# Optimization experiments

Hardware: AMD Instinct MI355X
Metric: run time of the kernel (lower is better)

Reference implementation:

```python
import jax, jax.numpy as jnp
import numpy as np

M, N, K, B = 256, 1024, 16, 16384
P = [50] * K          # topk support size per iteration
EPS = 0.1             # epsilon in g(x)


def g(x):
    # adaptive threshold gate: 1 / (x/eps + 1)
    return 1.0 / (x / EPS + 1.0)


def soft_threshold(x, theta, p):
    # x, theta: [N, B]; keep entries above the p-th largest |x| per column,
    # soft-threshold the rest.
    abs_ = jnp.abs(x)
    st = jnp.sign(x) * jnp.maximum(abs_ - theta, 0.0)
    if p == 0:
        return st
    topk_vals, _ = jax.lax.top_k(abs_.T, p)      # [B, p], sorted descending
    thr = topk_vals[:, -1]                        # p-th largest per column -> [B]
    keep = (abs_ > thr[None, :]).astype(x.dtype)  # strict >, matching torch
    return keep * x + (1.0 - keep) * st


def setup_inputs() -> dict:
    key = jax.random.key(0)
    k1, k2, k3 = jax.random.split(key, 3)
    y = jax.random.normal(k1, (B, M), jnp.float32)
    phi = jax.random.normal(k2, (M, N), jnp.float32) / np.sqrt(M)
    W = jax.random.normal(k3, (M, N), jnp.float32) / np.sqrt(M)
    gamma = jnp.full((K,), 0.5, jnp.float32)
    theta = jnp.full((K,), 0.5, jnp.float32)
    info = jnp.zeros((1,), jnp.int32)  # unused by forward, pass-through arg
    return {"y": y, "phi": phi, "W": W, "gamma": gamma, "theta": theta, "info": info}


def reference(y, phi, W, gamma, theta, info):
    # y: [B, M]; phi, W: [M, N]; gamma, theta: [K]
    x = jnp.zeros((N, y.shape[0]), y.dtype)  # [N, B]
    yT = y.T                                  # [M, B]
    for i in range(K):
        c = W.T @ (phi @ x - yT)              # [N, B]
        th = theta[i] * g(jnp.abs(x))
        x = soft_threshold(x - gamma[i] * c, th, P[i])
    return (x.T, jnp.zeros((K, 1), x.dtype), jnp.zeros((K, 1), x.dtype))
```

## Files before the change

kernel.cpp:

```cpp
#include <hip/hip_runtime.h>
#include <hip/hip_bf16.h>
#include <cstdint>

#define NB 16384
#define NM 256
#define NN 1024
#define NITER 16
#define TOPK 50

typedef __attribute__((ext_vector_type(8))) short short8;
typedef __attribute__((ext_vector_type(4))) float f32x4;

__device__ inline unsigned short f2bf(float x) {
    unsigned u = __float_as_uint(x);
    return (unsigned short)((u + 0x7FFFu + ((u >> 16) & 1u)) >> 16);
}
__device__ inline float bf2f(unsigned short h) {
    return __uint_as_float(((unsigned)h) << 16);
}
__device__ inline void gload16(const void* g, void* lds) {
    __builtin_amdgcn_global_load_lds(
        (const __attribute__((address_space(1))) unsigned*)g,
        (__attribute__((address_space(3))) unsigned*)lds, 16, 0, 0);
}

__global__ __launch_bounds__(256) void split_phi_kernel(const float* __restrict__ phi,
                                                        unsigned short* __restrict__ h,
                                                        unsigned short* __restrict__ l) {
    int i = blockIdx.x * 256 + threadIdx.x;
    float v = phi[i];
    unsigned short hh = f2bf(v);
    h[i] = hh;
    l[i] = f2bf(v - bf2f(hh));
}

__global__ __launch_bounds__(256) void transpose_split_W(const float* __restrict__ W,
                                                         unsigned short* __restrict__ th,
                                                         unsigned short* __restrict__ tl) {
    __shared__ float tile[32][33];
    int n0 = blockIdx.x * 32;
    int m0 = blockIdx.y * 32;
    int tx = threadIdx.x;
    int ty = threadIdx.y;
    #pragma unroll
    for (int i = 0; i < 32; i += 8)
        tile[ty + i][tx] = W[(size_t)(m0 + ty + i) * NN + n0 + tx];
    __syncthreads();
    #pragma unroll
    for (int i = 0; i < 32; i += 8) {
        float v = tile[tx][ty + i];
        unsigned short hh = f2bf(v);
        size_t idx = (size_t)(n0 + ty + i) * NM + m0 + tx;
        th[idx] = hh;
        tl[idx] = f2bf(v - bf2f(hh));
    }
}

#define BM1 128
#define BN1 64
#define BK  32
__global__ __launch_bounds__(256) void gemm1_mfma(const unsigned short* __restrict__ Xh,
                                                  const unsigned short* __restrict__ Xl,
                                                  const unsigned short* __restrict__ Ph,
                                                  const unsigned short* __restrict__ Pl,
                                                  const float* __restrict__ y,
                                                  unsigned short* __restrict__ Rth,
                                                  unsigned short* __restrict__ Rtl) {
    __shared__ unsigned short sAh[BM1 * BK];
    __shared__ unsigned short sAl[BM1 * BK];
    __shared__ unsigned short sBh[BN1 * BK];
    __shared__ unsigned short sBl[BN1 * BK];

    const int tid = threadIdx.x, wave = tid >> 6, lane = tid & 63;
    const int b0 = blockIdx.x * BM1, n0 = blockIdx.y * BN1;
    const int wm = (wave & 1) * 64, wn = (wave >> 1) * 32;
    const int row16 = lane & 15, quad = lane >> 4;

    f32x4 acc[4][2];
    #pragma unroll
    for (int i = 0; i < 4; i++)
        #pragma unroll
        for (int j = 0; j < 2; j++) acc[i][j] = (f32x4){0.f, 0.f, 0.f, 0.f};

    for (int k0 = 0; k0 < NN; k0 += BK) {
        #pragma unroll
        for (int c = 0; c < 2; ++c) {
            int o = (wave * 2 + c) * 1024 + lane * 16;
            int row = o >> 6, colb = o & 63;
            size_t g = (size_t)(b0 + row) * NN + k0 + (colb >> 1);
            gload16(&Xh[g], (char*)sAh + o);
            gload16(&Xl[g], (char*)sAl + o);
        }
        {
            int o = wave * 1024 + lane * 16;
            int nrow = o >> 6, colb = o & 63;
            size_t g = (size_t)(n0 + nrow) * NN + k0 + (colb >> 1);
            gload16(&Ph[g], (char*)sBh + o);
            gload16(&Pl[g], (char*)sBl + o);
        }
        __syncthreads();
        short8 a[4], bh[2], bl[2];
        #pragma unroll
        for (int j = 0; j < 2; ++j) {
            int off = (wn + j * 16 + row16) * 64 + quad * 16;
            bh[j] = *(const short8*)((const char*)sBh + off);
            bl[j] = *(const short8*)((const char*)sBl + off);
        }
        #pragma unroll
        for (int i = 0; i < 4; ++i)
            a[i] = *(const short8*)((const char*)sAh + (wm + i * 16 + row16) * 64 + quad * 16);
        #pragma unroll
        for (int i = 0; i < 4; ++i)
            #pragma unroll
            for (int j = 0; j < 2; ++j) {
                acc[i][j] = __builtin_amdgcn_mfma_f32_16x16x32_bf16(a[i], bh[j], acc[i][j], 0, 0, 0);
                acc[i][j] = __builtin_amdgcn_mfma_f32_16x16x32_bf16(a[i], bl[j], acc[i][j], 0, 0, 0);
            }
        #pragma unroll
        for (int i = 0; i < 4; ++i)
            a[i] = *(const short8*)((const char*)sAl + (wm + i * 16 + row16) * 64 + quad * 16);
        #pragma unroll
        for (int i = 0; i < 4; ++i)
            #pragma unroll
            for (int j = 0; j < 2; ++j)
                acc[i][j] = __builtin_amdgcn_mfma_f32_16x16x32_bf16(a[i], bh[j], acc[i][j], 0, 0, 0);
        __syncthreads();
    }
    #pragma unroll
    for (int i = 0; i < 4; ++i)
        #pragma unroll
        for (int j = 0; j < 2; ++j)
            #pragma unroll
            for (int r = 0; r < 4; ++r) {
                int gm = b0 + wm + i * 16 + quad * 4 + r;
                int gn = n0 + wn + j * 16 + row16;
                size_t idx = (size_t)gm * NM + gn;
                float v = acc[i][j][r] - y[idx];
                unsigned short h = f2bf(v);
                Rth[idx] = h;
                Rtl[idx] = f2bf(v - bf2f(h));
            }
}

#define BM2 128
#define BN2 128
__global__ __launch_bounds__(256) void gemm2_mfma(const unsigned short* __restrict__ Rth,
                                                  const unsigned short* __restrict__ Rtl,
                                                  const unsigned short* __restrict__ Wth,
                                                  const unsigned short* __restrict__ Wtl,
                                                  const unsigned short* __restrict__ Xh,
                                                  const unsigned short* __restrict__ Xl,
                                                  const float* __restrict__ gamma,
                                                  int it,
                                                  float* __restrict__ V) {
    __shared__ unsigned short sAh[BM2 * BK];
    __shared__ unsigned short sAl[BM2 * BK];
    __shared__ unsigned short sBh[BN2 * BK];
    __shared__ unsigned short sBl[BN2 * BK];

    const int tid = threadIdx.x, wave = tid >> 6, lane = tid & 63;
    const int b0 = blockIdx.x * BM2, n0 = blockIdx.y * BN2;
    const int wm = (wave & 1) * 64, wn = (wave >> 1) * 64;
    const int row16 = lane & 15, quad = lane >> 4;

    f32x4 acc[4][4];
    #pragma unroll
    for (int i = 0; i < 4; i++)
        #pragma unroll
        for (int j = 0; j < 4; j++) acc[i][j] = (f32x4){0.f, 0.f, 0.f, 0.f};

    for (int k0 = 0; k0 < NM; k0 += BK) {
        #pragma unroll
        for (int c = 0; c < 2; ++c) {
            int o = (wave * 2 + c) * 1024 + lane * 16;
            int row = o >> 6, colb = o & 63;
            size_t gA = (size_t)(b0 + row) * NM + k0 + (colb >> 1);
            gload16(&Rth[gA], (char*)sAh + o);
            gload16(&Rtl[gA], (char*)sAl + o);
            size_t gB = (size_t)(n0 + row) * NM + k0 + (colb >> 1);
            gload16(&Wth[gB], (char*)sBh + o);
            gload16(&Wtl[gB], (char*)sBl + o);
        }
        __syncthreads();
        short8 a[4], bh[4], bl[4];
        #pragma unroll
        for (int j = 0; j < 4; ++j) {
            int off = (wn + j * 16 + row16) * 64 + quad * 16;
            bh[j] = *(const short8*)((const char*)sBh + off);
            bl[j] = *(const short8*)((const char*)sBl + off);
        }
        #pragma unroll
        for (int i = 0; i < 4; ++i)
            a[i] = *(const short8*)((const char*)sAh + (wm + i * 16 + row16) * 64 + quad * 16);
        #pragma unroll
        for (int i = 0; i < 4; ++i)
            #pragma unroll
            for (int j = 0; j < 4; ++j) {
                acc[i][j] = __builtin_amdgcn_mfma_f32_16x16x32_bf16(a[i], bh[j], acc[i][j], 0, 0, 0);
                acc[i][j] = __builtin_amdgcn_mfma_f32_16x16x32_bf16(a[i], bl[j], acc[i][j], 0, 0, 0);
            }
        #pragma unroll
        for (int i = 0; i < 4; ++i)
            a[i] = *(const short8*)((const char*)sAl + (wm + i * 16 + row16) * 64 + quad * 16);
        #pragma unroll
        for (int i = 0; i < 4; ++i)
            #pragma unroll
            for (int j = 0; j < 4; ++j)
                acc[i][j] = __builtin_amdgcn_mfma_f32_16x16x32_bf16(a[i], bh[j], acc[i][j], 0, 0, 0);
        __syncthreads();
    }
    float gm = gamma[it];
    #pragma unroll
    for (int i = 0; i < 4; ++i)
        #pragma unroll
        for (int j = 0; j < 4; ++j)
            #pragma unroll
            for (int r = 0; r < 4; ++r) {
                int gmr = b0 + wm + i * 16 + quad * 4 + r;
                int gn = n0 + wn + j * 16 + row16;
                size_t idx = (size_t)gmr * NN + gn;
                float xo = bf2f(Xh[idx]) + bf2f(Xl[idx]);
                V[idx] = xo - gm * acc[i][j][r];
            }
}

__global__ __launch_bounds__(256) void update_kernel(const float* __restrict__ V,
                                                     unsigned short* __restrict__ Xh,
                                                     unsigned short* __restrict__ Xl,
                                                     const float* __restrict__ theta,
                                                     int it,
                                                     float* __restrict__ out) {
    __shared__ unsigned hist[2048];
    __shared__ unsigned wtot[4];
    __shared__ unsigned s_bin;
    __shared__ unsigned s_r2;
    __shared__ unsigned s_cnt;
    __shared__ unsigned s_T;
    __shared__ unsigned s_low[1024];

    const int b = blockIdx.x, tid = threadIdx.x;
    const int lane = tid & 63, wave = tid >> 6;
    const size_t base = (size_t)b * NN + tid * 4;

    float4 vv = *reinterpret_cast<const float4*>(&V[base]);
    float v[4] = {vv.x, vv.y, vv.z, vv.w};
    unsigned u[4];
    #pragma unroll
    for (int j = 0; j < 4; j++) u[j] = __float_as_uint(fabsf(v[j]));

    uint4 z4 = {0u, 0u, 0u, 0u};
    reinterpret_cast<uint4*>(hist)[tid] = z4;
    reinterpret_cast<uint4*>(hist)[tid + 256] = z4;
    if (tid == 0) s_cnt = 0;
    __syncthreads();

    #pragma unroll
    for (int j = 0; j < 4; j++) atomicAdd(&hist[u[j] >> 20], 1u);
    __syncthreads();

    unsigned loc[8];
    uint4 h0 = reinterpret_cast<const uint4*>(hist)[tid * 2];
    uint4 h1 = reinterpret_cast<const uint4*>(hist)[tid * 2 + 1];
    loc[0] = h0.x; loc[1] = h0.y; loc[2] = h0.z; loc[3] = h0.w;
    loc[4] = h1.x; loc[5] = h1.y; loc[6] = h1.z; loc[7] = h1.w;
    unsigned lsum = 0;
    #pragma unroll
    for (int i = 0; i < 8; i++) lsum += loc[i];

    unsigned s = lsum;
    #pragma unroll
    for (int off = 1; off < 64; off <<= 1) {
        unsigned o = __shfl_down(s, off, 64);
        if (lane + off < 64) s += o;
    }
    if (lane == 0) wtot[wave] = s;
    __syncthreads();
    unsigned after_wave = 0;
    #pragma unroll
    for (int w = 0; w < 4; ++w)
        if (w > wave) after_wave += wtot[w];
    unsigned S_incl = s + after_wave;
    unsigned run = S_incl - lsum;

    const unsigned r = TOPK;
    #pragma unroll
    for (int i = 7; i >= 0; --i) {
        unsigned sufThis = run + loc[i];
        if (sufThis >= r && run < r) { s_bin = tid * 8 + i; s_r2 = r - run; }
        run = sufThis;
    }
    __syncthreads();
    const unsigned bin = s_bin, r2 = s_r2;

    #pragma unroll
    for (int j = 0; j < 4; j++) {
        if ((u[j] >> 20) == bin) {
            unsigned p = atomicAdd(&s_cnt, 1u);
            s_low[p] = u[j] & 0xFFFFFu;
        }
    }
    __syncthreads();
    const unsigned c = s_cnt;
    for (unsigned p = tid; p < c; p += 256) {
        unsigned x = s_low[p];
        unsigned cg = 0, ce = 0;
        for (unsigned q = 0; q < c; ++q) {
            unsigned yq = s_low[q];
            cg += (yq > x);
            ce += (yq == x);
        }
        if (cg < r2 && cg + ce >= r2) s_T = (bin << 20) | x;
    }
    __syncthreads();
    const unsigned T = s_T;

    float thv = theta[it];
    ushort4 xh4 = *reinterpret_cast<const ushort4*>(&Xh[base]);
    ushort4 xl4 = *reinterpret_cast<const ushort4*>(&Xl[base]);
    const unsigned short* xhp = reinterpret_cast<const unsigned short*>(&xh4);
    const unsigned short* xlp = reinterpret_cast<const unsigned short*>(&xl4);
    ushort4 nh4, nl4;
    unsigned short* nhp = reinterpret_cast<unsigned short*>(&nh4);
    unsigned short* nlp = reinterpret_cast<unsigned short*>(&nl4);
    float ov[4];
    #pragma unroll
    for (int j = 0; j < 4; j++) {
        float xo = bf2f(xhp[j]) + bf2f(xlp[j]);
        float th = thv / (10.0f * fabsf(xo) + 1.0f);
        float a = fabsf(v[j]);
        float st = copysignf(fmaxf(a - th, 0.0f), v[j]);
        float outv = (u[j] > T) ? v[j] : st;
        unsigned short h = f2bf(outv);
        nhp[j] = h;
        nlp[j] = f2bf(outv - bf2f(h));
        ov[j] = outv;
    }
    *reinterpret_cast<ushort4*>(&Xh[base]) = nh4;
    *reinterpret_cast<ushort4*>(&Xl[base]) = nl4;
    if (it == NITER - 1)
        *reinterpret_cast<float4*>(&out[base]) = *reinterpret_cast<float4*>(ov);
}

__global__ void tail_kernel(float* __restrict__ out) {
    if (threadIdx.x < 32) out[(size_t)NB * NN + threadIdx.x] = 0.0f;
}

extern "C" void kernel_launch(void* const* d_in, const int* in_sizes, int n_in,
                              void* d_out, int out_size, void* d_ws, size_t ws_size,
                              hipStream_t stream) {
    const float* y     = (const float*)d_in[0];
    const float* phi   = (const float*)d_in[1];
    const float* W     = (const float*)d_in[2];
    const float* gamma = (const float*)d_in[3];
    const float* theta = (const float*)d_in[4];
    float* out = (float*)d_out;

    char* ws = (char*)d_ws;
    size_t off = 0;
    unsigned short* Xh  = (unsigned short*)(ws + off); off += (size_t)NB * NN * 2;
    unsigned short* Xl  = (unsigned short*)(ws + off); off += (size_t)NB * NN * 2;
    unsigned short* Rth = (unsigned short*)(ws + off); off += (size_t)NB * NM * 2;
    unsigned short* Rtl = (unsigned short*)(ws + off); off += (size_t)NB * NM * 2;
    unsigned short* Ph  = (unsigned short*)(ws + off); off += (size_t)NM * NN * 2;
    unsigned short* Pl  = (unsigned short*)(ws + off); off += (size_t)NM * NN * 2;
    unsigned short* Wth = (unsigned short*)(ws + off); off += (size_t)NN * NM * 2;
    unsigned short* Wtl = (unsigned short*)(ws + off); off += (size_t)NN * NM * 2;
    float* V = out;

    hipMemsetAsync(Xh, 0, (size_t)NB * NN * 2, stream);
    hipMemsetAsync(Xl, 0, (size_t)NB * NN * 2, stream);
    split_phi_kernel<<<(NM * NN) / 256, 256, 0, stream>>>(phi, Ph, Pl);
    transpose_split_W<<<dim3(NN / 32, NM / 32), dim3(32, 8), 0, stream>>>(W, Wth, Wtl);

    for (int it = 0; it < NITER; ++it) {
        gemm1_mfma<<<dim3(NB / BM1, NM / BN1), 256, 0, stream>>>(Xh, Xl, Ph, Pl, y, Rth, Rtl);
        gemm2_mfma<<<dim3(NB / BM2, NN / BN2), 256, 0, stream>>>(Rth, Rtl, Wth, Wtl, Xh, Xl,
                                                                 gamma, it, V);
        update_kernel<<<NB, 256, 0, stream>>>(V, Xh, Xl, theta, it, out);
    }
    tail_kernel<<<1, 32, 0, stream>>>(out);
}
```

Before: 2.037 ms.

## Fuse all ALISTA iterations into one persistent kernel with LDS-resident state

Replaces the per-iteration gemm1, gemm2 and top-k update kernels with a single kernel. Each block owns 32 batch rows and keeps their split-bf16 state X and residual R in swizzled LDS across all 16 iterations. The top-k threshold is found by a 4-pass radix select over packed 16-bit histograms instead of a 2048-bin histogram plus a quadratic refinement. This removes the global round trips for X, R and V and the 48 kernel launches. The cost is 160KB of LDS per block, phi and W tiles read straight from global/L2 without LDS staging, and only 512 blocks of work.

```diff
diff --git a/kernel.cpp b/kernel.cpp
--- a/kernel.cpp
+++ b/kernel.cpp
@@ -1,5 +1,4 @@
 #include <hip/hip_runtime.h>
-#include <hip/hip_bf16.h>
 #include <cstdint>
 
 #define NB 16384
@@ -7,6 +6,8 @@
 #define NN 1024
 #define NITER 16
 #define TOPK 50
+#define BMROW 32
+#define NBLKS (NB / BMROW)
 
 typedef __attribute__((ext_vector_type(8))) short short8;
 typedef __attribute__((ext_vector_type(4))) float f32x4;
@@ -17,11 +18,6 @@
 }
 __device__ inline float bf2f(unsigned short h) {
     return __uint_as_float(((unsigned)h) << 16);
-}
-__device__ inline void gload16(const void* g, void* lds) {
-    __builtin_amdgcn_global_load_lds(
-        (const __attribute__((address_space(1))) unsigned*)g,
-        (__attribute__((address_space(3))) unsigned*)lds, 16, 0, 0);
 }
 
 __global__ __launch_bounds__(256) void split_phi_kernel(const float* __restrict__ phi,
@@ -56,289 +52,238 @@
     }
 }
 
-#define BM1 128
-#define BN1 64
-#define BK  32
-__global__ __launch_bounds__(256) void gemm1_mfma(const unsigned short* __restrict__ Xh,
-                                                  const unsigned short* __restrict__ Xl,
-                                                  const unsigned short* __restrict__ Ph,
-                                                  const unsigned short* __restrict__ Pl,
-                                                  const float* __restrict__ y,
-                                                  unsigned short* __restrict__ Rth,
-                                                  unsigned short* __restrict__ Rtl) {
-    __shared__ unsigned short sAh[BM1 * BK];
-    __shared__ unsigned short sAl[BM1 * BK];
-    __shared__ unsigned short sBh[BN1 * BK];
-    __shared__ unsigned short sBl[BN1 * BK];
-
-    const int tid = threadIdx.x, wave = tid >> 6, lane = tid & 63;
-    const int b0 = blockIdx.x * BM1, n0 = blockIdx.y * BN1;
-    const int wm = (wave & 1) * 64, wn = (wave >> 1) * 32;
-    const int row16 = lane & 15, quad = lane >> 4;
-
-    f32x4 acc[4][2];
-    #pragma unroll
-    for (int i = 0; i < 4; i++)
-        #pragma unroll
-        for (int j = 0; j < 2; j++) acc[i][j] = (f32x4){0.f, 0.f, 0.f, 0.f};
-
-    for (int k0 = 0; k0 < NN; k0 += BK) {
-        #pragma unroll
-        for (int c = 0; c < 2; ++c) {
-            int o = (wave * 2 + c) * 1024 + lane * 16;
-            int row = o >> 6, colb = o & 63;
-            size_t g = (size_t)(b0 + row) * NN + k0 + (colb >> 1);
-            gload16(&Xh[g], (char*)sAh + o);
-            gload16(&Xl[g], (char*)sAl + o);
+#define XH_OFF 0
+#define XL_OFF 65536
+#define RH_OFF 131072
+#define RL_OFF 147456
+#define HSTRIDE 132
+#define PREF_OFF (131072 + 4224 * 4)
+#define RK_OFF (PREF_OFF + 128)
+
+__global__ __launch_bounds__(512, 2) void alista_fused(
+        const unsigned short* __restrict__ Ph, const unsigned short* __restrict__ Pl,
+        const unsigned short* __restrict__ Wth, const unsigned short* __restrict__ Wtl,
+        const float* __restrict__ y, const float* __restrict__ gamma,
+        const float* __restrict__ theta, float* __restrict__ out) {
+    extern __shared__ char lds[];
+    const int tid = threadIdx.x;
+    const int w = tid >> 6;
+    const int lane = tid & 63;
+    const int qd = lane >> 4;
+    const int r16 = lane & 15;
+    const int gb0 = blockIdx.x * BMROW;
+    const unsigned swzA = (unsigned)((r16 & 7) << 4);
+
+    {
+        uint32_t* p = (uint32_t*)lds;
+        #pragma unroll
+        for (int i = 0; i < 64; ++i) p[tid + i * 512] = 0u;
+    }
+    __syncthreads();
+
+    const unsigned short* pPh0 = Ph + (size_t)(w * 32 + r16) * NN + qd * 8;
+    const unsigned short* pPh1 = pPh0 + 16 * NN;
+    const unsigned short* pPl0 = Pl + (size_t)(w * 32 + r16) * NN + qd * 8;
+    const unsigned short* pPl1 = pPl0 + 16 * NN;
+    const size_t wn0 = (size_t)(w * 128 + r16) * NM + qd * 8;
+
+    for (int it = 0; it < NITER; ++it) {
+        const float gm = gamma[it];
+        const float thv = theta[it];
+
+        f32x4 acc1[2][2];
+        #pragma unroll
+        for (int i = 0; i < 2; ++i)
+            #pragma unroll
+            for (int j = 0; j < 2; ++j) acc1[i][j] = (f32x4){0.f, 0.f, 0.f, 0.f};
+
+        #pragma unroll 4
+        for (int k = 0; k < 32; ++k) {
+            short8 bh[2], bl[2], ah[2], al[2];
+            bh[0] = *(const short8*)(pPh0 + k * 32);
+            bh[1] = *(const short8*)(pPh1 + k * 32);
+            bl[0] = *(const short8*)(pPl0 + k * 32);
+            bl[1] = *(const short8*)(pPl1 + k * 32);
+            const unsigned mo = ((unsigned)(k * 64 + qd * 16)) ^ swzA;
+            ah[0] = *(const short8*)(lds + XH_OFF + r16 * 2048 + mo);
+            ah[1] = *(const short8*)(lds + XH_OFF + (r16 + 16) * 2048 + mo);
+            al[0] = *(const short8*)(lds + XL_OFF + r16 * 2048 + mo);
+            al[1] = *(const short8*)(lds + XL_OFF + (r16 + 16) * 2048 + mo);
+            #pragma unroll
+            for (int bb = 0; bb < 2; ++bb)
+                #pragma unroll
+                for (int m = 0; m < 2; ++m) {
+                    acc1[bb][m] = __builtin_amdgcn_mfma_f32_16x16x32_bf16(ah[bb], bh[m], acc1[bb][m], 0, 0, 0);
+                    acc1[bb][m] = __builtin_amdgcn_mfma_f32_16x16x32_bf16(ah[bb], bl[m], acc1[bb][m], 0, 0, 0);
+                    acc1[bb][m] = __builtin_amdgcn_mfma_f32_16x16x32_bf16(al[bb], bh[m], acc1[bb][m], 0, 0, 0);
+                }
         }
-        {
-            int o = wave * 1024 + lane * 16;
-            int nrow = o >> 6, colb = o & 63;
-            size_t g = (size_t)(n0 + nrow) * NN + k0 + (colb >> 1);
-            gload16(&Ph[g], (char*)sBh + o);
-            gload16(&Pl[g], (char*)sBl + o);
+        #pragma unroll
+        for (int bb = 0; bb < 2; ++bb)
+            #pragma unroll
+            for (int m = 0; m < 2; ++m) {
+                const int gmn = w * 32 + m * 16 + r16;
+                #pragma unroll
+                for (int r = 0; r < 4; ++r) {
+                    const int b = bb * 16 + qd * 4 + r;
+                    float v = acc1[bb][m][r] - y[(size_t)(gb0 + b) * NM + gmn];
+                    unsigned short h = f2bf(v);
+                    const unsigned mb = ((unsigned)(gmn * 2)) ^ ((unsigned)((b & 7) << 4));
+                    *(unsigned short*)(lds + RH_OFF + b * 512 + mb) = h;
+                    *(unsigned short*)(lds + RL_OFF + b * 512 + mb) = f2bf(v - bf2f(h));
+                }
+            }
+        __syncthreads();
+
+        f32x4 acc2[2][8];
+        #pragma unroll
+        for (int i = 0; i < 2; ++i)
+            #pragma unroll
+            for (int j = 0; j < 8; ++j) acc2[i][j] = (f32x4){0.f, 0.f, 0.f, 0.f};
+
+        #pragma unroll 2
+        for (int k = 0; k < 8; ++k) {
+            short8 wh[8], wl[8];
+            #pragma unroll
+            for (int j = 0; j < 8; ++j) {
+                wh[j] = *(const short8*)(Wth + wn0 + j * 4096 + k * 32);
+                wl[j] = *(const short8*)(Wtl + wn0 + j * 4096 + k * 32);
+            }
+            const unsigned mo = ((unsigned)(k * 64 + qd * 16)) ^ swzA;
+            short8 ah[2], al[2];
+            ah[0] = *(const short8*)(lds + RH_OFF + r16 * 512 + mo);
+            ah[1] = *(const short8*)(lds + RH_OFF + (r16 + 16) * 512 + mo);
+            al[0] = *(const short8*)(lds + RL_OFF + r16 * 512 + mo);
+            al[1] = *(const short8*)(lds + RL_OFF + (r16 + 16) * 512 + mo);
+            #pragma unroll
+            for (int bb = 0; bb < 2; ++bb)
+                #pragma unroll
+                for (int j = 0; j < 8; ++j) {
+                    acc2[bb][j] = __builtin_amdgcn_mfma_f32_16x16x32_bf16(ah[bb], wh[j], acc2[bb][j], 0, 0, 0);
+                    acc2[bb][j] = __builtin_amdgcn_mfma_f32_16x16x32_bf16(ah[bb], wl[j], acc2[bb][j], 0, 0, 0);
+                    acc2[bb][j] = __builtin_amdgcn_mfma_f32_16x16x32_bf16(al[bb], wh[j], acc2[bb][j], 0, 0, 0);
+                }
         }
+
+        #pragma unroll
+        for (int bb = 0; bb < 2; ++bb)
+            #pragma unroll
+            for (int j = 0; j < 8; ++j) {
+                const int n = w * 128 + j * 16 + r16;
+                #pragma unroll
+                for (int r = 0; r < 4; ++r) {
+                    const int b = bb * 16 + qd * 4 + r;
+                    const unsigned nb2 = ((unsigned)(n * 2)) ^ ((unsigned)((b & 7) << 4));
+                    float xo = bf2f(*(const unsigned short*)(lds + XH_OFF + b * 2048 + nb2)) +
+                               bf2f(*(const unsigned short*)(lds + XL_OFF + b * 2048 + nb2));
+                    acc2[bb][j][r] = xo - gm * acc2[bb][j][r];
+                }
+            }
         __syncthreads();
-        short8 a[4], bh[2], bl[2];
-        #pragma unroll
-        for (int j = 0; j < 2; ++j) {
-            int off = (wn + j * 16 + row16) * 64 + quad * 16;
-            bh[j] = *(const short8*)((const char*)sBh + off);
-            bl[j] = *(const short8*)((const char*)sBl + off);
+
+        uint32_t* hist = (uint32_t*)(lds + RH_OFF);
+        uint32_t* prefA = (uint32_t*)(lds + PREF_OFF);
+        uint32_t* rkA = (uint32_t*)(lds + RK_OFF);
+        #pragma unroll
+        for (int i = 0; i < 9; ++i) {
+            int idx = tid + i * 512;
+            if (idx < 32 * HSTRIDE) hist[idx] = 0u;
         }
-        #pragma unroll
-        for (int i = 0; i < 4; ++i)
-            a[i] = *(const short8*)((const char*)sAh + (wm + i * 16 + row16) * 64 + quad * 16);
-        #pragma unroll
-        for (int i = 0; i < 4; ++i)
-            #pragma unroll
-            for (int j = 0; j < 2; ++j) {
-                acc[i][j] = __builtin_amdgcn_mfma_f32_16x16x32_bf16(a[i], bh[j], acc[i][j], 0, 0, 0);
-                acc[i][j] = __builtin_amdgcn_mfma_f32_16x16x32_bf16(a[i], bl[j], acc[i][j], 0, 0, 0);
-            }
-        #pragma unroll
-        for (int i = 0; i < 4; ++i)
-            a[i] = *(const short8*)((const char*)sAl + (wm + i * 16 + row16) * 64 + quad * 16);
-        #pragma unroll
-        for (int i = 0; i < 4; ++i)
-            #pragma unroll
-            for (int j = 0; j < 2; ++j)
-                acc[i][j] = __builtin_amdgcn_mfma_f32_16x16x32_bf16(a[i], bh[j], acc[i][j], 0, 0, 0);
+        if (tid < 32) { prefA[tid] = 0u; rkA[tid] = TOPK; }
+        __syncthreads();
+
+        const int srow = w * 4 + qd;
+        #pragma unroll
+        for (int pass = 0; pass < 4; ++pass) {
+            const int s = (pass == 0) ? 23 : (pass == 1) ? 15 : (pass == 2) ? 7 : 0;
+            const int sTop = (pass == 0) ? 31 : (pass == 1) ? 23 : (pass == 2) ? 15 : 7;
+            const unsigned bmask = (pass == 3) ? 0x7Fu : 0xFFu;
+            unsigned prefs[2][4];
+            #pragma unroll
+            for (int bb = 0; bb < 2; ++bb)
+                #pragma unroll
+                for (int r = 0; r < 4; ++r) prefs[bb][r] = prefA[bb * 16 + qd * 4 + r];
+            #pragma unroll
+            for (int bb = 0; bb < 2; ++bb)
+                #pragma unroll
+                for (int j = 0; j < 8; ++j)
+                    #pragma unroll
+                    for (int r = 0; r < 4; ++r) {
+                        unsigned u = __float_as_uint(acc2[bb][j][r]) & 0x7FFFFFFFu;
+                        if ((u >> sTop) == (prefs[bb][r] >> sTop)) {
+                            unsigned bin = (u >> s) & bmask;
+                            atomicAdd(&hist[(bb * 16 + qd * 4 + r) * HSTRIDE + (bin >> 1)],
+                                      1u << ((bin & 1) * 16));
+                        }
+                    }
+            __syncthreads();
+            unsigned cnt[16];
+            unsigned lsum = 0;
+            #pragma unroll
+            for (int i = 0; i < 8; ++i) {
+                unsigned wd = hist[srow * HSTRIDE + r16 * 8 + i];
+                cnt[2 * i] = wd & 0xFFFFu;
+                cnt[2 * i + 1] = wd >> 16;
+                lsum += cnt[2 * i] + cnt[2 * i + 1];
+            }
+            unsigned S = lsum;
+            #pragma unroll
+            for (int off = 1; off < 16; off <<= 1) {
+                unsigned o = (unsigned)__shfl_down((int)S, off, 16);
+                if (r16 + off < 16) S += o;
+            }
+            const unsigned rk = rkA[srow];
+            const unsigned pOld = prefA[srow];
+            unsigned run = S - lsum;
+            #pragma unroll
+            for (int i = 15; i >= 0; --i) {
+                unsigned tot = run + cnt[i];
+                if (run < rk && tot >= rk) {
+                    prefA[srow] = pOld | (((unsigned)(r16 * 16 + i)) << s);
+                    rkA[srow] = rk - run;
+                }
+                run = tot;
+            }
+            __syncthreads();
+            if (pass < 3) {
+                #pragma unroll
+                for (int i = 0; i < 9; ++i) {
+                    int idx = tid + i * 512;
+                    if (idx < 32 * HSTRIDE) hist[idx] = 0u;
+                }
+                __syncthreads();
+            }
+        }
+
+        unsigned Ts[2][4];
+        #pragma unroll
+        for (int bb = 0; bb < 2; ++bb)
+            #pragma unroll
+            for (int r = 0; r < 4; ++r) Ts[bb][r] = prefA[bb * 16 + qd * 4 + r];
+        #pragma unroll
+        for (int bb = 0; bb < 2; ++bb)
+            #pragma unroll
+            for (int j = 0; j < 8; ++j) {
+                const int n = w * 128 + j * 16 + r16;
+                #pragma unroll
+                for (int r = 0; r < 4; ++r) {
+                    const int b = bb * 16 + qd * 4 + r;
+                    const unsigned nb2 = ((unsigned)(n * 2)) ^ ((unsigned)((b & 7) << 4));
+                    float xo = bf2f(*(const unsigned short*)(lds + XH_OFF + b * 2048 + nb2)) +
+                               bf2f(*(const unsigned short*)(lds + XL_OFF + b * 2048 + nb2));
+                    float v = acc2[bb][j][r];
+                    float th = thv / (10.0f * fabsf(xo) + 1.0f);
+                    float st = copysignf(fmaxf(fabsf(v) - th, 0.0f), v);
+                    unsigned u = __float_as_uint(v) & 0x7FFFFFFFu;
+                    float outv = (u > Ts[bb][r]) ? v : st;
+                    unsigned short h = f2bf(outv);
+                    *(unsigned short*)(lds + XH_OFF + b * 2048 + nb2) = h;
+                    *(unsigned short*)(lds + XL_OFF + b * 2048 + nb2) = f2bf(outv - bf2f(h));
+                    if (it == NITER - 1) out[(size_t)(gb0 + b) * NN + n] = outv;
+                }
+            }
         __syncthreads();
     }
-    #pragma unroll
-    for (int i = 0; i < 4; ++i)
-        #pragma unroll
-        for (int j = 0; j < 2; ++j)
-            #pragma unroll
-            for (int r = 0; r < 4; ++r) {
-                int gm = b0 + wm + i * 16 + quad * 4 + r;
-                int gn = n0 + wn + j * 16 + row16;
-                size_t idx = (size_t)gm * NM + gn;
-                float v = acc[i][j][r] - y[idx];
-                unsigned short h = f2bf(v);
-                Rth[idx] = h;
-                Rtl[idx] = f2bf(v - bf2f(h));
-            }
-}
-
-#define BM2 128
-#define BN2 128
-__global__ __launch_bounds__(256) void gemm2_mfma(const unsigned short* __restrict__ Rth,
-                                                  const unsigned short* __restrict__ Rtl,
-                                                  const unsigned short* __restrict__ Wth,
-                                                  const unsigned short* __restrict__ Wtl,
-                                                  const unsigned short* __restrict__ Xh,
-                                                  const unsigned short* __restrict__ Xl,
-                                                  const float* __restrict__ gamma,
-                                                  int it,
-                                                  float* __restrict__ V) {
-    __shared__ unsigned short sAh[BM2 * BK];
-    __shared__ unsigned short sAl[BM2 * BK];
-    __shared__ unsigned short sBh[BN2 * BK];
-    __shared__ unsigned short sBl[BN2 * BK];
-
-    const int tid = threadIdx.x, wave = tid >> 6, lane = tid & 63;
-    const int b0 = blockIdx.x * BM2, n0 = blockIdx.y * BN2;
-    const int wm = (wave & 1) * 64, wn = (wave >> 1) * 64;
-    const int row16 = lane & 15, quad = lane >> 4;
-
-    f32x4 acc[4][4];
-    #pragma unroll
-    for (int i = 0; i < 4; i++)
-        #pragma unroll
-        for (int j = 0; j < 4; j++) acc[i][j] = (f32x4){0.f, 0.f, 0.f, 0.f};
-
-    for (int k0 = 0; k0 < NM; k0 += BK) {
-        #pragma unroll
-        for (int c = 0; c < 2; ++c) {
-            int o = (wave * 2 + c) * 1024 + lane * 16;
-            int row = o >> 6, colb = o & 63;
-            size_t gA = (size_t)(b0 + row) * NM + k0 + (colb >> 1);
-            gload16(&Rth[gA], (char*)sAh + o);
-            gload16(&Rtl[gA], (char*)sAl + o);
-            size_t gB = (size_t)(n0 + row) * NM + k0 + (colb >> 1);
-            gload16(&Wth[gB], (char*)sBh + o);
-            gload16(&Wtl[gB], (char*)sBl + o);
-        }
-        __syncthreads();
-        short8 a[4], bh[4], bl[4];
-        #pragma unroll
-        for (int j = 0; j < 4; ++j) {
-            int off = (wn + j * 16 + row16) * 64 + quad * 16;
-            bh[j] = *(const short8*)((const char*)sBh + off);
-            bl[j] = *(const short8*)((const char*)sBl + off);
-        }
-        #pragma unroll
-        for (int i = 0; i < 4; ++i)
-            a[i] = *(const short8*)((const char*)sAh + (wm + i * 16 + row16) * 64 + quad * 16);
-        #pragma unroll
-        for (int i = 0; i < 4; ++i)
-            #pragma unroll
-            for (int j = 0; j < 4; ++j) {
-                acc[i][j] = __builtin_amdgcn_mfma_f32_16x16x32_bf16(a[i], bh[j], acc[i][j], 0, 0, 0);
-                acc[i][j] = __builtin_amdgcn_mfma_f32_16x16x32_bf16(a[i], bl[j], acc[i][j], 0, 0, 0);
-            }
-        #pragma unroll
-        for (int i = 0; i < 4; ++i)
-            a[i] = *(const short8*)((const char*)sAl + (wm + i * 16 + row16) * 64 + quad * 16);
-        #pragma unroll
-        for (int i = 0; i < 4; ++i)
-            #pragma unroll
-            for (int j = 0; j < 4; ++j)
-                acc[i][j] = __builtin_amdgcn_mfma_f32_16x16x32_bf16(a[i], bh[j], acc[i][j], 0, 0, 0);
-        __syncthreads();
-    }
-    float gm = gamma[it];
-    #pragma unroll
-    for (int i = 0; i < 4; ++i)
-        #pragma unroll
-        for (int j = 0; j < 4; ++j)
-            #pragma unroll
-            for (int r = 0; r < 4; ++r) {
-                int gmr = b0 + wm + i * 16 + quad * 4 + r;
-                int gn = n0 + wn + j * 16 + row16;
-                size_t idx = (size_t)gmr * NN + gn;
-                float xo = bf2f(Xh[idx]) + bf2f(Xl[idx]);
-                V[idx] = xo - gm * acc[i][j][r];
-            }
-}
-
-__global__ __launch_bounds__(256) void update_kernel(const float* __restrict__ V,
-                                                     unsigned short* __restrict__ Xh,
-                                                     unsigned short* __restrict__ Xl,
-                                                     const float* __restrict__ theta,
-                                                     int it,
-                                                     float* __restrict__ out) {
-    __shared__ unsigned hist[2048];
-    __shared__ unsigned wtot[4];
-    __shared__ unsigned s_bin;
-    __shared__ unsigned s_r2;
-    __shared__ unsigned s_cnt;
-    __shared__ unsigned s_T;
-    __shared__ unsigned s_low[1024];
-
-    const int b = blockIdx.x, tid = threadIdx.x;
-    const int lane = tid & 63, wave = tid >> 6;
-    const size_t base = (size_t)b * NN + tid * 4;
-
-    float4 vv = *reinterpret_cast<const float4*>(&V[base]);
-    float v[4] = {vv.x, vv.y, vv.z, vv.w};
-    unsigned u[4];
-    #pragma unroll
-    for (int j = 0; j < 4; j++) u[j] = __float_as_uint(fabsf(v[j]));
-
-    uint4 z4 = {0u, 0u, 0u, 0u};
-    reinterpret_cast<uint4*>(hist)[tid] = z4;
-    reinterpret_cast<uint4*>(hist)[tid + 256] = z4;
-    if (tid == 0) s_cnt = 0;
-    __syncthreads();
-
-    #pragma unroll
-    for (int j = 0; j < 4; j++) atomicAdd(&hist[u[j] >> 20], 1u);
-    __syncthreads();
-
-    unsigned loc[8];
-    uint4 h0 = reinterpret_cast<const uint4*>(hist)[tid * 2];
-    uint4 h1 = reinterpret_cast<const uint4*>(hist)[tid * 2 + 1];
-    loc[0] = h0.x; loc[1] = h0.y; loc[2] = h0.z; loc[3] = h0.w;
-    loc[4] = h1.x; loc[5] = h1.y; loc[6] = h1.z; loc[7] = h1.w;
-    unsigned lsum = 0;
-    #pragma unroll
-    for (int i = 0; i < 8; i++) lsum += loc[i];
-
-    unsigned s = lsum;
-    #pragma unroll
-    for (int off = 1; off < 64; off <<= 1) {
-        unsigned o = __shfl_down(s, off, 64);
-        if (lane + off < 64) s += o;
-    }
-    if (lane == 0) wtot[wave] = s;
-    __syncthreads();
-    unsigned after_wave = 0;
-    #pragma unroll
-    for (int w = 0; w < 4; ++w)
-        if (w > wave) after_wave += wtot[w];
-    unsigned S_incl = s + after_wave;
-    unsigned run = S_incl - lsum;
-
-    const unsigned r = TOPK;
-    #pragma unroll
-    for (int i = 7; i >= 0; --i) {
-        unsigned sufThis = run + loc[i];
-        if (sufThis >= r && run < r) { s_bin = tid * 8 + i; s_r2 = r - run; }
-        run = sufThis;
-    }
-    __syncthreads();
-    const unsigned bin = s_bin, r2 = s_r2;
-
-    #pragma unroll
-    for (int j = 0; j < 4; j++) {
-        if ((u[j] >> 20) == bin) {
-            unsigned p = atomicAdd(&s_cnt, 1u);
-            s_low[p] = u[j] & 0xFFFFFu;
-        }
-    }
-    __syncthreads();
-    const unsigned c = s_cnt;
-    for (unsigned p = tid; p < c; p += 256) {
-        unsigned x = s_low[p];
-        unsigned cg = 0, ce = 0;
-        for (unsigned q = 0; q < c; ++q) {
-            unsigned yq = s_low[q];
-            cg += (yq > x);
-            ce += (yq == x);
-        }
-        if (cg < r2 && cg + ce >= r2) s_T = (bin << 20) | x;
-    }
-    __syncthreads();
-    const unsigned T = s_T;
-
-    float thv = theta[it];
-    ushort4 xh4 = *reinterpret_cast<const ushort4*>(&Xh[base]);
-    ushort4 xl4 = *reinterpret_cast<const ushort4*>(&Xl[base]);
-    const unsigned short* xhp = reinterpret_cast<const unsigned short*>(&xh4);
-    const unsigned short* xlp = reinterpret_cast<const unsigned short*>(&xl4);
-    ushort4 nh4, nl4;
-    unsigned short* nhp = reinterpret_cast<unsigned short*>(&nh4);
-    unsigned short* nlp = reinterpret_cast<unsigned short*>(&nl4);
-    float ov[4];
-    #pragma unroll
-    for (int j = 0; j < 4; j++) {
-        float xo = bf2f(xhp[j]) + bf2f(xlp[j]);
-        float th = thv / (10.0f * fabsf(xo) + 1.0f);
-        float a = fabsf(v[j]);
-        float st = copysignf(fmaxf(a - th, 0.0f), v[j]);
-        float outv = (u[j] > T) ? v[j] : st;
-        unsigned short h = f2bf(outv);
-        nhp[j] = h;
-        nlp[j] = f2bf(outv - bf2f(h));
-        ov[j] = outv;
-    }
-    *reinterpret_cast<ushort4*>(&Xh[base]) = nh4;
-    *reinterpret_cast<ushort4*>(&Xl[base]) = nl4;
-    if (it == NITER - 1)
-        *reinterpret_cast<float4*>(&out[base]) = *reinterpret_cast<float4*>(ov);
 }
 
 __global__ void tail_kernel(float* __restrict__ out) {
@@ -357,26 +302,20 @@
 
     char* ws = (char*)d_ws;
     size_t off = 0;
-    unsigned short* Xh  = (unsigned short*)(ws + off); off += (size_t)NB * NN * 2;
-    unsigned short* Xl  = (unsigned short*)(ws + off); off += (size_t)NB * NN * 2;
-    unsigned short* Rth = (unsigned short*)(ws + off); off += (size_t)NB * NM * 2;
-    unsigned short* Rtl = (unsigned short*)(ws + off); off += (size_t)NB * NM * 2;
     unsigned short* Ph  = (unsigned short*)(ws + off); off += (size_t)NM * NN * 2;
     unsigned short* Pl  = (unsigned short*)(ws + off); off += (size_t)NM * NN * 2;
     unsigned short* Wth = (unsigned short*)(ws + off); off += (size_t)NN * NM * 2;
     unsigned short* Wtl = (unsigned short*)(ws + off); off += (size_t)NN * NM * 2;
-    float* V = out;
-
-    hipMemsetAsync(Xh, 0, (size_t)NB * NN * 2, stream);
-    hipMemsetAsync(Xl, 0, (size_t)NB * NN * 2, stream);
+
+    static int attr_done = 0;
+    if (!attr_done) {
+        (void)hipFuncSetAttribute(reinterpret_cast<const void*>(alista_fused),
+                                  hipFuncAttributeMaxDynamicSharedMemorySize, 163840);
+        attr_done = 1;
+    }
+
     split_phi_kernel<<<(NM * NN) / 256, 256, 0, stream>>>(phi, Ph, Pl);
     transpose_split_W<<<dim3(NN / 32, NM / 32), dim3(32, 8), 0, stream>>>(W, Wth, Wtl);
-
-    for (int it = 0; it < NITER; ++it) {
-        gemm1_mfma<<<dim3(NB / BM1, NM / BN1), 256, 0, stream>>>(Xh, Xl, Ph, Pl, y, Rth, Rtl);
-        gemm2_mfma<<<dim3(NB / BM2, NN / BN2), 256, 0, stream>>>(Rth, Rtl, Wth, Wtl, Xh, Xl,
-                                                                 gamma, it, V);
-        update_kernel<<<NB, 256, 0, stream>>>(V, Xh, Xl, theta, it, out);
-    }
+    alista_fused<<<NBLKS, 512, 163840, stream>>>(Ph, Pl, Wth, Wtl, y, gamma, theta, out);
     tail_kernel<<<1, 32, 0, stream>>>(out);
 }
```

Result: slower. 3.766 ms (+84.9%).

## Peel first iteration using zero initial state and move x reads into update

Applied to the files above, without the earlier changes.

Since x starts at zero, the first residual is just -y, so the first gemm1 and the Xh/Xl memsets are replaced by a small elementwise kernel that splits -y into bf16 hi/lo. gemm2 now stores the raw product, and the update kernel combines x, gamma and the product itself, reading x once instead of in both gemm2's epilogue and update. A templated FIRST variant skips loading x on iteration zero. This trades a little extra kernel specialization for less redundant work and memory traffic.

```diff
diff --git a/kernel.cpp b/kernel.cpp
--- a/kernel.cpp
+++ b/kernel.cpp
@@ -1,5 +1,4 @@
 #include <hip/hip_runtime.h>
-#include <hip/hip_bf16.h>
 #include <cstdint>
 
 #define NB 16384
@@ -54,6 +53,26 @@
         th[idx] = hh;
         tl[idx] = f2bf(v - bf2f(hh));
     }
+}
+
+__global__ __launch_bounds__(256) void rt_init_kernel(const float* __restrict__ y,
+                                                      unsigned short* __restrict__ Rth,
+                                                      unsigned short* __restrict__ Rtl) {
+    size_t i = ((size_t)blockIdx.x * 256 + threadIdx.x) * 4;
+    float4 v4 = *reinterpret_cast<const float4*>(&y[i]);
+    float vv[4] = {v4.x, v4.y, v4.z, v4.w};
+    ushort4 h4, l4;
+    unsigned short* hp = reinterpret_cast<unsigned short*>(&h4);
+    unsigned short* lp = reinterpret_cast<unsigned short*>(&l4);
+    #pragma unroll
+    for (int e = 0; e < 4; ++e) {
+        float v = -vv[e];
+        unsigned short h = f2bf(v);
+        hp[e] = h;
+        lp[e] = f2bf(v - bf2f(h));
+    }
+    *reinterpret_cast<ushort4*>(&Rth[i]) = h4;
+    *reinterpret_cast<ushort4*>(&Rtl[i]) = l4;
 }
 
 #define BM1 128
@@ -148,11 +167,7 @@
                                                   const unsigned short* __restrict__ Rtl,
                                                   const unsigned short* __restrict__ Wth,
                                                   const unsigned short* __restrict__ Wtl,
-                                                  const unsigned short* __restrict__ Xh,
-                                                  const unsigned short* __restrict__ Xl,
-                                                  const float* __restrict__ gamma,
-                                                  int it,
-                                                  float* __restrict__ V) {
+                                                  float* __restrict__ C) {
     __shared__ unsigned short sAh[BM2 * BK];
     __shared__ unsigned short sAl[BM2 * BK];
     __shared__ unsigned short sBh[BN2 * BK];
@@ -209,7 +224,6 @@
                 acc[i][j] = __builtin_amdgcn_mfma_f32_16x16x32_bf16(a[i], bh[j], acc[i][j], 0, 0, 0);
         __syncthreads();
     }
-    float gm = gamma[it];
     #pragma unroll
     for (int i = 0; i < 4; ++i)
         #pragma unroll
@@ -218,15 +232,15 @@
             for (int r = 0; r < 4; ++r) {
                 int gmr = b0 + wm + i * 16 + quad * 4 + r;
                 int gn = n0 + wn + j * 16 + row16;
-                size_t idx = (size_t)gmr * NN + gn;
-                float xo = bf2f(Xh[idx]) + bf2f(Xl[idx]);
-                V[idx] = xo - gm * acc[i][j][r];
+                C[(size_t)gmr * NN + gn] = acc[i][j][r];
             }
 }
 
-__global__ __launch_bounds__(256) void update_kernel(const float* __restrict__ V,
+template <int FIRST>
+__global__ __launch_bounds__(256) void update_kernel(const float* __restrict__ C,
                                                      unsigned short* __restrict__ Xh,
                                                      unsigned short* __restrict__ Xl,
+                                                     const float* __restrict__ gamma,
                                                      const float* __restrict__ theta,
                                                      int it,
                                                      float* __restrict__ out) {
@@ -241,12 +255,31 @@
     const int b = blockIdx.x, tid = threadIdx.x;
     const int lane = tid & 63, wave = tid >> 6;
     const size_t base = (size_t)b * NN + tid * 4;
-
-    float4 vv = *reinterpret_cast<const float4*>(&V[base]);
-    float v[4] = {vv.x, vv.y, vv.z, vv.w};
+    const float gm = gamma[it];
+
+    float4 cc = *reinterpret_cast<const float4*>(&C[base]);
+    float c4[4] = {cc.x, cc.y, cc.z, cc.w};
+
+    ushort4 xh4, xl4;
+    float xo[4];
+    if (FIRST) {
+        xo[0] = xo[1] = xo[2] = xo[3] = 0.0f;
+    } else {
+        xh4 = *reinterpret_cast<const ushort4*>(&Xh[base]);
+        xl4 = *reinterpret_cast<const ushort4*>(&Xl[base]);
+        const unsigned short* xhp = reinterpret_cast<const unsigned short*>(&xh4);
+        const unsigned short* xlp = reinterpret_cast<const unsigned short*>(&xl4);
+        #pragma unroll
+        for (int j = 0; j < 4; j++) xo[j] = bf2f(xhp[j]) + bf2f(xlp[j]);
+    }
+
+    float v[4];
     unsigned u[4];
     #pragma unroll
-    for (int j = 0; j < 4; j++) u[j] = __float_as_uint(fabsf(v[j]));
+    for (int j = 0; j < 4; j++) {
+        v[j] = xo[j] - gm * c4[j];
+        u[j] = __float_as_uint(fabsf(v[j]));
+    }
 
     uint4 z4 = {0u, 0u, 0u, 0u};
     reinterpret_cast<uint4*>(hist)[tid] = z4;
@@ -315,18 +348,13 @@
     const unsigned T = s_T;
 
     float thv = theta[it];
-    ushort4 xh4 = *reinterpret_cast<const ushort4*>(&Xh[base]);
-    ushort4 xl4 = *reinterpret_cast<const ushort4*>(&Xl[base]);
-    const unsigned short* xhp = reinterpret_cast<const unsigned short*>(&xh4);
-    const unsigned short* xlp = reinterpret_cast<const unsigned short*>(&xl4);
     ushort4 nh4, nl4;
     unsigned short* nhp = reinterpret_cast<unsigned short*>(&nh4);
     unsigned short* nlp = reinterpret_cast<unsigned short*>(&nl4);
     float ov[4];
     #pragma unroll
     for (int j = 0; j < 4; j++) {
-        float xo = bf2f(xhp[j]) + bf2f(xlp[j]);
-        float th = thv / (10.0f * fabsf(xo) + 1.0f);
+        float th = thv / (10.0f * fabsf(xo[j]) + 1.0f);
         float a = fabsf(v[j]);
         float st = copysignf(fmaxf(a - th, 0.0f), v[j]);
         float outv = (u[j] > T) ? v[j] : st;
@@ -365,18 +393,19 @@
     unsigned short* Pl  = (unsigned short*)(ws + off); off += (size_t)NM * NN * 2;
     unsigned short* Wth = (unsigned short*)(ws + off); off += (size_t)NN * NM * 2;
     unsigned short* Wtl = (unsigned short*)(ws + off); off += (size_t)NN * NM * 2;
-    float* V = out;
-
-    hipMemsetAsync(Xh, 0, (size_t)NB * NN * 2, stream);
-    hipMemsetAsync(Xl, 0, (size_t)NB * NN * 2, stream);
+    float* C = out;
+
     split_phi_kernel<<<(NM * NN) / 256, 256, 0, stream>>>(phi, Ph, Pl);
     transpose_split_W<<<dim3(NN / 32, NM / 32), dim3(32, 8), 0, stream>>>(W, Wth, Wtl);
 
-    for (int it = 0; it < NITER; ++it) {
+    rt_init_kernel<<<(NB * NM) / (256 * 4), 256, 0, stream>>>(y, Rth, Rtl);
+    gemm2_mfma<<<dim3(NB / BM2, NN / BN2), 256, 0, stream>>>(Rth, Rtl, Wth, Wtl, C);
+    update_kernel<1><<<NB, 256, 0, stream>>>(C, Xh, Xl, gamma, theta, 0, out);
+
+    for (int it = 1; it < NITER; ++it) {
         gemm1_mfma<<<dim3(NB / BM1, NM / BN1), 256, 0, stream>>>(Xh, Xl, Ph, Pl, y, Rth, Rtl);
-        gemm2_mfma<<<dim3(NB / BM2, NN / BN2), 256, 0, stream>>>(Rth, Rtl, Wth, Wtl, Xh, Xl,
-                                                                 gamma, it, V);
-        update_kernel<<<NB, 256, 0, stream>>>(V, Xh, Xl, theta, it, out);
+        gemm2_mfma<<<dim3(NB / BM2, NN / BN2), 256, 0, stream>>>(Rth, Rtl, Wth, Wtl, C);
+        update_kernel<0><<<NB, 256, 0, stream>>>(C, Xh, Xl, gamma, theta, it, out);
     }
     tail_kernel<<<1, 32, 0, stream>>>(out);
 }
```

Measured after the change: 1.863 ms. 8.6% less time.
